# Kernel optimization log

Measured on AMD Instinct MI355X. Metric: run time of the kernel, lower is better.

Reference implementation:

```python
import jax, jax.numpy as jnp
import numpy as np

H, D, EF, NT, ET = 4, 32, 32, 4, 8
N, E = 100000, 1600000
NEG_SLOPE = 0.2


def setup_inputs() -> dict:
    key = jax.random.key(0)
    ks = jax.random.split(key, 11)
    return {
        "feat": jax.random.normal(ks[0], (N, H * D), jnp.float32),
        "fc": jax.random.normal(ks[1], (NT, H, D), jnp.float32) * 0.1,
        "edge_emb": jax.random.normal(ks[2], (ET, EF), jnp.float32),
        "W_e": jax.random.normal(ks[3], (H * EF, EF), jnp.float32) * 0.1,
        "attn_l": jax.random.normal(ks[4], (1, H, D), jnp.float32) * 0.1,
        "attn_r": jax.random.normal(ks[5], (1, H, D), jnp.float32) * 0.1,
        "attn_e": jax.random.normal(ks[6], (1, H, EF), jnp.float32) * 0.1,
        "node_types": jax.random.randint(ks[7], (N,), 0, NT, jnp.int32),
        "e_feat": jax.random.randint(ks[8], (E,), 0, ET, jnp.int32),
        "src": jax.random.randint(ks[9], (E,), 0, N, jnp.int32),
        "dst": jax.random.randint(ks[10], (E,), 0, N, jnp.int32),
    }


def reference(feat, fc, edge_emb, W_e, attn_l, attn_r, attn_e, node_types, e_feat, src, dst):
    n = feat.shape[0]
    h = feat.reshape(n, H, D)                      # [N,H,D] (h_src == h_dst)
    fs = h * fc[node_types]                        # per-node-type scaling, feat_src == feat_dst

    # edge-type embedding path: Embedding -> Linear(edge_feats, H*edge_feats) -> attn_e score
    emb = (edge_emb @ W_e.T).reshape(ET, H, EF)    # [ET,H,EF]
    ee = (emb * attn_e).sum(-1)[e_feat]            # [E,H]

    el = (fs * attn_l).sum(-1)                     # [N,H]
    er = (fs * attn_r).sum(-1)                     # [N,H]
    e = jax.nn.leaky_relu(el[src] + er[dst] + ee, NEG_SLOPE)  # [E,H]

    # edge_softmax: segment softmax over destination node
    m = jax.ops.segment_max(e, dst, num_segments=n)           # [N,H]
    ex = jnp.exp(e - m[dst])
    s = jax.ops.segment_sum(ex, dst, num_segments=n)          # [N,H]
    a = ex / s[dst]                                            # [E,H]

    # u_mul_e + sum aggregation
    msg = fs[src] * a[:, :, None]                              # [E,H,D]
    rst = jax.ops.segment_sum(msg, dst, num_segments=n)       # [N,H,D]

    rst = rst + h                                              # residual (Identity, in==out feats)
    return rst, a[:, :, None]
```

## Files before the change

kernel.cpp:

```cpp
#include <hip/hip_runtime.h>
#include <stdint.h>

namespace {
constexpr int kH = 4, kD = 32, kEF = 32, kNT = 4, kET = 8;
constexpr int kHD = kH * kD;
constexpr float kNegSlope = 0.2f;
constexpr int kNB = 782;
constexpr int kHB = 512;

using f32x2 = __attribute__((ext_vector_type(2))) float;

__device__ __forceinline__ float lrelu(float x) { return x > 0.f ? x : kNegSlope * x; }

__global__ void __launch_bounds__(256) k_init(
    const float* __restrict__ feat, const float* __restrict__ fc,
    const float* __restrict__ edge_emb, const float* __restrict__ W_e,
    const float* __restrict__ attn_l, const float* __restrict__ attn_r,
    const float* __restrict__ attn_e, const int* __restrict__ node_types,
    float* __restrict__ el, float* __restrict__ er, uint8_t* __restrict__ fs,
    float* __restrict__ ee_tab, int N) {
  if (blockIdx.x == 0 && threadIdx.x < kET * kH) {
    int et = threadIdx.x / kH, h = threadIdx.x % kH;
    float acc = 0.f;
    for (int f = 0; f < kEF; ++f) {
      const float* wrow = W_e + (h * kEF + f) * kEF;
      const float* erow = edge_emb + et * kEF;
      float emb = 0.f;
      for (int k = 0; k < kEF; ++k) emb += erow[k] * wrow[k];
      acc += emb * attn_e[h * kEF + f];
    }
    ee_tab[et * kH + h] = acc;
  }
  int gid = blockIdx.x * blockDim.x + threadIdx.x;
  int node = gid >> 6;
  int lane = threadIdx.x & 63;
  if (node >= N) return;
  int nt = node_types[node];
  float2 f2 = *(const float2*)(feat + node * kHD + lane * 2);
  float2 c2 = *(const float2*)(fc + nt * kHD + lane * 2);
  float2 al = *(const float2*)(attn_l + lane * 2);
  float2 ar = *(const float2*)(attn_r + lane * 2);
  float fx = f2.x * c2.x, fy = f2.y * c2.y;
  float nx = __shfl_down(fx, 1);
  float ny = __shfl_down(fy, 1);
  if ((lane & 1) == 0) {
    int w = __builtin_amdgcn_cvt_pk_fp8_f32(fx, fy, 0, false);
    w = __builtin_amdgcn_cvt_pk_fp8_f32(nx, ny, w, true);
    *(int*)(fs + (size_t)node * kHD + lane * 2) = w;
  }
  float pl = fx * al.x + fy * al.y;
  float pr = fx * ar.x + fy * ar.y;
#pragma unroll
  for (int off = 1; off < 16; off <<= 1) {
    pl += __shfl_xor(pl, off);
    pr += __shfl_xor(pr, off);
  }
  if ((lane & 15) == 0) {
    int h = lane >> 4;
    el[node * kH + h] = pl;
    er[node * kH + h] = pr;
  }
}

__global__ void __launch_bounds__(256) k_hist(const int* __restrict__ dst,
                                              int* __restrict__ partial, int E) {
  __shared__ int h[kNB];
  for (int i = threadIdx.x; i < kNB; i += 256) h[i] = 0;
  __syncthreads();
  int per = (E + gridDim.x - 1) / gridDim.x;
  int e0 = blockIdx.x * per;
  int e1 = min(e0 + per, E);
  for (int i = e0 + threadIdx.x; i < e1; i += 256) atomicAdd(&h[dst[i] >> 7], 1);
  __syncthreads();
  for (int i = threadIdx.x; i < kNB; i += 256) partial[blockIdx.x * kNB + i] = h[i];
}

__global__ void __launch_bounds__(256) k_scanA(int* __restrict__ partial,
                                               int* __restrict__ btot) {
  __shared__ int bufa[kHB], bufb[kHB];
  int b = blockIdx.x, t = threadIdx.x;
  bufa[t] = partial[t * kNB + b];
  bufa[t + 256] = partial[(t + 256) * kNB + b];
  __syncthreads();
  int* cur = bufa;
  int* nxt = bufb;
  for (int off = 1; off < kHB; off <<= 1) {
    for (int i = t; i < kHB; i += 256) nxt[i] = cur[i] + (i >= off ? cur[i - off] : 0);
    __syncthreads();
    int* sw = cur; cur = nxt; nxt = sw;
  }
  partial[t * kNB + b] = t ? cur[t - 1] : 0;
  partial[(t + 256) * kNB + b] = cur[t + 255];
  if (t == 0) btot[b] = cur[kHB - 1];
}

__global__ void __launch_bounds__(1024) k_scanB(const int* __restrict__ btot,
                                                int* __restrict__ bbase) {
  __shared__ int bufa[1024], bufb[1024];
  int t = threadIdx.x;
  bufa[t] = (t < kNB) ? btot[t] : 0;
  __syncthreads();
  int* cur = bufa;
  int* nxt = bufb;
  for (int off = 1; off < 1024; off <<= 1) {
    nxt[t] = cur[t] + (t >= off ? cur[t - off] : 0);
    __syncthreads();
    int* sw = cur; cur = nxt; nxt = sw;
  }
  if (t < kNB) bbase[t] = t ? cur[t - 1] : 0;
  if (t == kNB - 1) bbase[kNB] = cur[t];
}

__global__ void __launch_bounds__(256) k_scatter2(
    const int* __restrict__ dst, const int* __restrict__ src,
    const int* __restrict__ e_feat, const int* __restrict__ partial,
    const int* __restrict__ bbase, int* __restrict__ tmp, int E) {
  __shared__ int h[kNB];
  for (int i = threadIdx.x; i < kNB; i += 256) h[i] = 0;
  __syncthreads();
  int per = (E + gridDim.x - 1) / gridDim.x;
  int e0 = blockIdx.x * per;
  int e1 = min(e0 + per, E);
  const int* myrow = partial + blockIdx.x * kNB;
  for (int i = e0 + threadIdx.x; i < e1; i += 256) {
    int d = dst[i];
    int b = d >> 7;
    int lr = atomicAdd(&h[b], 1);
    int pos = bbase[b] + myrow[b] + lr;
    tmp[pos] = src[i] | (e_feat[i] << 17) | ((d & 127) << 20);
  }
}

__global__ void __launch_bounds__(256) k_build(const int* __restrict__ bbase,
                                               const int* __restrict__ tmp,
                                               int* __restrict__ ptr,
                                               int* __restrict__ csr, int N, int E) {
  __shared__ int fh[128], fb[128], sc[128];
  int b = blockIdx.x, t = threadIdx.x;
  int s0 = bbase[b], s1 = bbase[b + 1];
  if (t < 128) fh[t] = 0;
  __syncthreads();
  for (int j = s0 + t; j < s1; j += 256) atomicAdd(&fh[tmp[j] >> 20], 1);
  __syncthreads();
  if (t < 128) sc[t] = fh[t];
  __syncthreads();
  for (int off = 1; off < 128; off <<= 1) {
    int v = 0;
    if (t < 128 && t >= off) v = sc[t - off];
    __syncthreads();
    if (t < 128) sc[t] += v;
    __syncthreads();
  }
  if (t < 128) {
    fb[t] = sc[t] - fh[t];
    int d = (b << 7) + t;
    if (d < N) ptr[d] = s0 + fb[t];
    fh[t] = 0;
  }
  if (b == gridDim.x - 1 && t == 0) ptr[N] = E;
  __syncthreads();
  for (int j = s0 + t; j < s1; j += 256) {
    int v = tmp[j];
    int dl = v >> 20;
    int r = atomicAdd(&fh[dl], 1);
    csr[s0 + fb[dl] + r] = v & 0xFFFFF;
  }
}

__global__ void __launch_bounds__(256) k_fused(
    const uint8_t* __restrict__ fs, const float* __restrict__ feat,
    const float* __restrict__ el, const float* __restrict__ er,
    const float* __restrict__ ee_tab, const int* __restrict__ ptr,
    const int* __restrict__ csr, float* __restrict__ rst,
    float* __restrict__ rinv_buf, int N) {
  __shared__ __align__(16) float ee_sh[kET * kH];
  if (threadIdx.x < kET * kH) ee_sh[threadIdx.x] = ee_tab[threadIdx.x];
  __syncthreads();
  int lane = threadIdx.x & 63;
  int node = blockIdx.x * (blockDim.x >> 6) + (threadIdx.x >> 6);
  if (node >= N) return;
  int start = ptr[node], end = ptr[node + 1];

  int g = lane >> 3;
  int q = lane & 7;
  int head = q >> 1;
  float er_h = er[node * kH + head];

  float sm = 0.f;
  float acc[16];
#pragma unroll
  for (int k = 0; k < 16; ++k) acc[k] = 0.f;

  for (int j = start + g; j < end; j += 8) {
    int pk = csr[j];
    int s = pk & 0x1FFFF;
    int et = (pk >> 17) & 7;
    float e_h = lrelu(el[s * kH + head] + er_h + ee_sh[et * kH + head]);
    float ex = __expf(e_h);
    sm += ex;
    int4 w = *(const int4*)(fs + (size_t)s * kHD + q * 16);
#pragma unroll
    for (int c = 0; c < 4; ++c) {
      int wc = c == 0 ? w.x : c == 1 ? w.y : c == 2 ? w.z : w.w;
      f32x2 lo = __builtin_amdgcn_cvt_pk_f32_fp8(wc, false);
      f32x2 hi = __builtin_amdgcn_cvt_pk_f32_fp8(wc, true);
      acc[c * 4 + 0] += ex * lo.x;
      acc[c * 4 + 1] += ex * lo.y;
      acc[c * 4 + 2] += ex * hi.x;
      acc[c * 4 + 3] += ex * hi.y;
    }
  }
  sm += __shfl_xor(sm, 8);
  sm += __shfl_xor(sm, 16);
  sm += __shfl_xor(sm, 32);
#pragma unroll
  for (int k = 0; k < 16; ++k) {
    acc[k] += __shfl_xor(acc[k], 8);
    acc[k] += __shfl_xor(acc[k], 16);
    acc[k] += __shfl_xor(acc[k], 32);
  }
  float rinv = sm > 0.f ? 1.f / sm : 0.f;

  if (g == 0) {
    const float* fr = feat + node * kHD + q * 16;
    float* out = rst + node * kHD + q * 16;
#pragma unroll
    for (int r = 0; r < 4; ++r) {
      float4 o;
      o.x = acc[r * 4 + 0] * rinv + fr[r * 4 + 0];
      o.y = acc[r * 4 + 1] * rinv + fr[r * 4 + 1];
      o.z = acc[r * 4 + 2] * rinv + fr[r * 4 + 2];
      o.w = acc[r * 4 + 3] * rinv + fr[r * 4 + 3];
      *(float4*)(out + r * 4) = o;
    }
    if ((q & 1) == 0) rinv_buf[node * kH + head] = rinv;
  }
}

__global__ void k_post(const int* __restrict__ src, const int* __restrict__ dst,
                       const int* __restrict__ e_feat, const float* __restrict__ el,
                       const float* __restrict__ er, const float* __restrict__ ee_tab,
                       const float* __restrict__ rinv_buf, float* __restrict__ out_a,
                       int E) {
  int i = blockIdx.x * blockDim.x + threadIdx.x;
  if (i >= E) return;
  int s = src[i], d = dst[i], et = e_feat[i];
  float4 elv = *(const float4*)(el + s * kH);
  float4 erv = *(const float4*)(er + d * kH);
  float4 ee = *(const float4*)(ee_tab + et * kH);
  float4 rv = *(const float4*)(rinv_buf + d * kH);
  float4 a;
  a.x = __expf(lrelu(elv.x + erv.x + ee.x)) * rv.x;
  a.y = __expf(lrelu(elv.y + erv.y + ee.y)) * rv.y;
  a.z = __expf(lrelu(elv.z + erv.z + ee.z)) * rv.z;
  a.w = __expf(lrelu(elv.w + erv.w + ee.w)) * rv.w;
  *(float4*)(out_a + (size_t)i * kH) = a;
}

}

extern "C" void kernel_launch(void* const* d_in, const int* in_sizes, int n_in,
                              void* d_out, int out_size, void* d_ws, size_t ws_size,
                              hipStream_t stream) {
  const float* feat = (const float*)d_in[0];
  const float* fc = (const float*)d_in[1];
  const float* edge_emb = (const float*)d_in[2];
  const float* W_e = (const float*)d_in[3];
  const float* attn_l = (const float*)d_in[4];
  const float* attn_r = (const float*)d_in[5];
  const float* attn_e = (const float*)d_in[6];
  const int* node_types = (const int*)d_in[7];
  const int* e_feat = (const int*)d_in[8];
  const int* src = (const int*)d_in[9];
  const int* dst = (const int*)d_in[10];
  int N = in_sizes[7];
  int E = in_sizes[8];

  char* ws = (char*)d_ws;
  size_t off = 0;
  auto alloc = [&](size_t bytes) -> void* {
    void* p = ws + off;
    off = (off + bytes + 255) & ~(size_t)255;
    return p;
  };
  float* ee_tab = (float*)alloc((size_t)kET * kH * sizeof(float));
  float* el = (float*)alloc((size_t)N * kH * sizeof(float));
  float* er = (float*)alloc((size_t)N * kH * sizeof(float));
  float* rinv_buf = (float*)alloc((size_t)N * kH * sizeof(float));
  uint8_t* fs = (uint8_t*)alloc((size_t)N * kHD * sizeof(uint8_t));
  int* partial = (int*)alloc((size_t)kHB * kNB * sizeof(int));
  int* btot = (int*)alloc((size_t)kNB * sizeof(int));
  int* bbase = (int*)alloc((size_t)(kNB + 1) * sizeof(int));
  int* ptr = (int*)alloc((size_t)(N + 1) * sizeof(int));
  int* tmp = (int*)alloc((size_t)E * sizeof(int));
  int* csr = (int*)alloc((size_t)E * sizeof(int));

  k_init<<<(N + 3) / 4, 256, 0, stream>>>(feat, fc, edge_emb, W_e, attn_l, attn_r,
                                          attn_e, node_types, el, er, fs, ee_tab, N);
  k_hist<<<kHB, 256, 0, stream>>>(dst, partial, E);
  k_scanA<<<kNB, 256, 0, stream>>>(partial, btot);
  k_scanB<<<1, 1024, 0, stream>>>(btot, bbase);
  k_scatter2<<<kHB, 256, 0, stream>>>(dst, src, e_feat, partial, bbase, tmp, E);
  k_build<<<kNB, 256, 0, stream>>>(bbase, tmp, ptr, csr, N, E);

  float* rst = (float*)d_out;
  float* out_a = (float*)d_out + (size_t)N * kHD;
  k_fused<<<(N + 3) / 4, 256, 0, stream>>>(fs, feat, el, er, ee_tab, ptr, csr, rst,
                                           rinv_buf, N);
  k_post<<<(E + 255) / 256, 256, 0, stream>>>(src, dst, e_feat, el, er, ee_tab,
                                              rinv_buf, out_a, E);
}
```

Baseline: 320.7 us.

## Prefetch gathered edges, reduce via shared memory, widen init loads

The aggregation loop is software-pipelined so the next edge's csr entry, el value, fp8 row and edge-type score are loaded while the current edge is accumulated. Accumulation uses packed float2 math. The 48 cross-lane shuffles for the final reduction are replaced by a padded shared-memory transpose, so all 64 lanes write the output with float2 stores. k_init now processes one node per 32 lanes with float4 loads and writes a full fp8 word without shuffles. The trade-offs are more registers, extra LDS use and a block-wide barrier, which means early-exit waves must stay alive until it.

Result: faster. 307.3 us (-4.2%).

```diff
diff --git a/kernel.cpp b/kernel.cpp
--- a/kernel.cpp
+++ b/kernel.cpp
@@ -7,6 +7,7 @@
 constexpr float kNegSlope = 0.2f;
 constexpr int kNB = 782;
 constexpr int kHB = 512;
+constexpr int kXP = 20;
 
 using f32x2 = __attribute__((ext_vector_type(2))) float;
 
@@ -32,31 +33,27 @@
     ee_tab[et * kH + h] = acc;
   }
   int gid = blockIdx.x * blockDim.x + threadIdx.x;
-  int node = gid >> 6;
-  int lane = threadIdx.x & 63;
+  int node = gid >> 5;
+  int lane = threadIdx.x & 31;
   if (node >= N) return;
   int nt = node_types[node];
-  float2 f2 = *(const float2*)(feat + node * kHD + lane * 2);
-  float2 c2 = *(const float2*)(fc + nt * kHD + lane * 2);
-  float2 al = *(const float2*)(attn_l + lane * 2);
-  float2 ar = *(const float2*)(attn_r + lane * 2);
-  float fx = f2.x * c2.x, fy = f2.y * c2.y;
-  float nx = __shfl_down(fx, 1);
-  float ny = __shfl_down(fy, 1);
-  if ((lane & 1) == 0) {
-    int w = __builtin_amdgcn_cvt_pk_fp8_f32(fx, fy, 0, false);
-    w = __builtin_amdgcn_cvt_pk_fp8_f32(nx, ny, w, true);
-    *(int*)(fs + (size_t)node * kHD + lane * 2) = w;
-  }
-  float pl = fx * al.x + fy * al.y;
-  float pr = fx * ar.x + fy * ar.y;
-#pragma unroll
-  for (int off = 1; off < 16; off <<= 1) {
+  float4 f4 = *(const float4*)(feat + (size_t)(node << 7) + lane * 4);
+  float4 c4 = *(const float4*)(fc + nt * kHD + lane * 4);
+  float4 al = *(const float4*)(attn_l + lane * 4);
+  float4 ar = *(const float4*)(attn_r + lane * 4);
+  float fx = f4.x * c4.x, fy = f4.y * c4.y, fz = f4.z * c4.z, fw = f4.w * c4.w;
+  int w = __builtin_amdgcn_cvt_pk_fp8_f32(fx, fy, 0, false);
+  w = __builtin_amdgcn_cvt_pk_fp8_f32(fz, fw, w, true);
+  *(int*)(fs + (size_t)(node << 7) + lane * 4) = w;
+  float pl = fx * al.x + fy * al.y + fz * al.z + fw * al.w;
+  float pr = fx * ar.x + fy * ar.y + fz * ar.z + fw * ar.w;
+#pragma unroll
+  for (int off = 1; off < 8; off <<= 1) {
     pl += __shfl_xor(pl, off);
     pr += __shfl_xor(pr, off);
   }
-  if ((lane & 15) == 0) {
-    int h = lane >> 4;
+  if ((lane & 7) == 0) {
+    int h = lane >> 3;
     el[node * kH + h] = pl;
     er[node * kH + h] = pr;
   }
@@ -173,67 +170,88 @@
     const float* __restrict__ ee_tab, const int* __restrict__ ptr,
     const int* __restrict__ csr, float* __restrict__ rst,
     float* __restrict__ rinv_buf, int N) {
-  __shared__ __align__(16) float ee_sh[kET * kH];
+  __shared__ float ee_sh[kET * kH];
+  __shared__ __align__(16) float xp[4][64 * kXP];
   if (threadIdx.x < kET * kH) ee_sh[threadIdx.x] = ee_tab[threadIdx.x];
   __syncthreads();
   int lane = threadIdx.x & 63;
-  int node = blockIdx.x * (blockDim.x >> 6) + (threadIdx.x >> 6);
-  if (node >= N) return;
-  int start = ptr[node], end = ptr[node + 1];
+  int wid = threadIdx.x >> 6;
+  int node = blockIdx.x * 4 + wid;
+  bool nvalid = node < N;
+  int nodec = nvalid ? node : 0;
+  int start = 0, end = 0;
+  if (nvalid) {
+    start = ptr[node];
+    end = ptr[node + 1];
+  }
 
   int g = lane >> 3;
   int q = lane & 7;
   int head = q >> 1;
-  float er_h = er[node * kH + head];
+  int qoff = q << 4;
+  float er_h = er[nodec * kH + head];
 
   float sm = 0.f;
-  float acc[16];
-#pragma unroll
-  for (int k = 0; k < 16; ++k) acc[k] = 0.f;
-
-  for (int j = start + g; j < end; j += 8) {
-    int pk = csr[j];
-    int s = pk & 0x1FFFF;
-    int et = (pk >> 17) & 7;
-    float e_h = lrelu(el[s * kH + head] + er_h + ee_sh[et * kH + head]);
-    float ex = __expf(e_h);
+  f32x2 acc[8];
+#pragma unroll
+  for (int k = 0; k < 8; ++k) acc[k] = (f32x2){0.f, 0.f};
+
+  int j = start + g;
+  int pk0 = csr[(j < end) ? j : 0];
+  int s0 = pk0 & 0x1FFFF;
+  float elv0 = el[(s0 << 2) + head];
+  int4 w0 = *(const int4*)(fs + (size_t)(s0 << 7) + qoff);
+  float ee0 = ee_sh[((pk0 >> 17) << 2) + head];
+  int pk1 = csr[(j + 8 < end) ? j + 8 : 0];
+
+  while (j < end) {
+    int s1 = pk1 & 0x1FFFF;
+    float elv1 = el[(s1 << 2) + head];
+    int4 w1 = *(const int4*)(fs + (size_t)(s1 << 7) + qoff);
+    float ee1 = ee_sh[((pk1 >> 17) << 2) + head];
+    int pk2 = csr[(j + 16 < end) ? j + 16 : 0];
+    float ex = __expf(lrelu(elv0 + er_h + ee0));
     sm += ex;
-    int4 w = *(const int4*)(fs + (size_t)s * kHD + q * 16);
+    f32x2 ex2 = {ex, ex};
 #pragma unroll
     for (int c = 0; c < 4; ++c) {
-      int wc = c == 0 ? w.x : c == 1 ? w.y : c == 2 ? w.z : w.w;
-      f32x2 lo = __builtin_amdgcn_cvt_pk_f32_fp8(wc, false);
-      f32x2 hi = __builtin_amdgcn_cvt_pk_f32_fp8(wc, true);
-      acc[c * 4 + 0] += ex * lo.x;
-      acc[c * 4 + 1] += ex * lo.y;
-      acc[c * 4 + 2] += ex * hi.x;
-      acc[c * 4 + 3] += ex * hi.y;
+      int wc = c == 0 ? w0.x : c == 1 ? w0.y : c == 2 ? w0.z : w0.w;
+      acc[2 * c + 0] += ex2 * __builtin_amdgcn_cvt_pk_f32_fp8(wc, false);
+      acc[2 * c + 1] += ex2 * __builtin_amdgcn_cvt_pk_f32_fp8(wc, true);
     }
-  }
+    elv0 = elv1;
+    w0 = w1;
+    ee0 = ee1;
+    pk1 = pk2;
+    j += 8;
+  }
+
   sm += __shfl_xor(sm, 8);
   sm += __shfl_xor(sm, 16);
   sm += __shfl_xor(sm, 32);
-#pragma unroll
-  for (int k = 0; k < 16; ++k) {
-    acc[k] += __shfl_xor(acc[k], 8);
-    acc[k] += __shfl_xor(acc[k], 16);
-    acc[k] += __shfl_xor(acc[k], 32);
-  }
   float rinv = sm > 0.f ? 1.f / sm : 0.f;
 
-  if (g == 0) {
-    const float* fr = feat + node * kHD + q * 16;
-    float* out = rst + node * kHD + q * 16;
-#pragma unroll
-    for (int r = 0; r < 4; ++r) {
-      float4 o;
-      o.x = acc[r * 4 + 0] * rinv + fr[r * 4 + 0];
-      o.y = acc[r * 4 + 1] * rinv + fr[r * 4 + 1];
-      o.z = acc[r * 4 + 2] * rinv + fr[r * 4 + 2];
-      o.w = acc[r * 4 + 3] * rinv + fr[r * 4 + 3];
-      *(float4*)(out + r * 4) = o;
-    }
-    if ((q & 1) == 0) rinv_buf[node * kH + head] = rinv;
+  float* row = &xp[wid][lane * kXP];
+#pragma unroll
+  for (int c = 0; c < 4; ++c) {
+    float4 v4 = {acc[2 * c].x, acc[2 * c].y, acc[2 * c + 1].x, acc[2 * c + 1].y};
+    *(float4*)(row + c * 4) = v4;
+  }
+  __syncthreads();
+  int qsrc = lane >> 3;
+  int coff = (lane & 7) * 2;
+  const float* base = &xp[wid][qsrc * kXP + coff];
+  f32x2 v = {0.f, 0.f};
+#pragma unroll
+  for (int gg = 0; gg < 8; ++gg) v += *(const f32x2*)(base + gg * 8 * kXP);
+
+  float rs = __shfl(rinv, (lane >> 4) << 1);
+  float rb = __shfl(rinv, lane << 1);
+  f32x2 f2 = *(const f32x2*)(feat + (size_t)(nodec << 7) + lane * 2);
+  f32x2 o = v * rs + f2;
+  if (nvalid) {
+    *(f32x2*)(rst + (size_t)(node << 7) + lane * 2) = o;
+    if (lane < kH) rinv_buf[node * kH + lane] = rb;
   }
 }
 
@@ -295,7 +313,7 @@
   int* tmp = (int*)alloc((size_t)E * sizeof(int));
   int* csr = (int*)alloc((size_t)E * sizeof(int));
 
-  k_init<<<(N + 3) / 4, 256, 0, stream>>>(feat, fc, edge_emb, W_e, attn_l, attn_r,
+  k_init<<<(N + 7) / 8, 256, 0, stream>>>(feat, fc, edge_emb, W_e, attn_l, attn_r,
                                           attn_e, node_types, el, er, fs, ee_tab, N);
   k_hist<<<kHB, 256, 0, stream>>>(dst, partial, E);
   k_scanA<<<kNB, 256, 0, stream>>>(partial, btot);
```
